# Optimization experiments

Measured on AMD Instinct MI355X. Metric: run time of the kernel, lower is better.

The kernel has to match this reference:

```python
import jax, jax.numpy as jnp
import numpy as np

N = 10000      # nodes
E = 160000     # edges
MUL = 64       # multiplicity of 0e and 1o in node feats / target
NATTR = 10     # number of element types (node_attrs one-hot width)
RDIM = 8       # radial (edge_feats) dim
NAVG = 16.0    # num_avg_neighbors
_INV3 = 0.5773502691896258  # CG coeff for 1o x 1o -> 0e (1/sqrt(3))


def setup_inputs() -> dict:
    key = jax.random.key(0)
    ks = jax.random.split(key, 20)
    return {
        "node_attrs": jax.random.uniform(ks[0], (N, NATTR), jnp.float32),
        "node_feats": jax.random.normal(ks[1], (N, 4 * MUL), jnp.float32),
        "edge_attrs_real": jax.random.normal(ks[2], (E, 4), jnp.float32),
        "edge_attrs_imag": jax.random.normal(ks[3], (E, 4), jnp.float32),
        "edge_feats": jax.random.normal(ks[4], (E, RDIM), jnp.float32),
        # linear_up (per-l internal weights)
        "W_up0": jax.random.normal(ks[5], (MUL, MUL), jnp.float32),
        "W_up1": jax.random.normal(ks[6], (MUL, MUL), jnp.float32),
        # conv_tp_weights MLP: [8, 64, 64, 64, 4*MUL]
        "M1": jax.random.normal(ks[7], (RDIM, 64), jnp.float32),
        "M2": jax.random.normal(ks[8], (64, 64), jnp.float32),
        "M3": jax.random.normal(ks[9], (64, 64), jnp.float32),
        "M4": jax.random.normal(ks[10], (64, 4 * MUL), jnp.float32),
        # linear: irreps_mid (128x0e+128x1o) -> irreps_nonlin (128x0e+64x1o)
        "W_lin_s": jax.random.normal(ks[11], (2 * MUL, 2 * MUL), jnp.float32),
        "W_lin_v": jax.random.normal(ks[12], (2 * MUL, MUL), jnp.float32),
        # skip_tp: FullyConnectedTensorProduct(node_feats, node_attrs -> irreps_nonlin)
        "W_sk_s": jax.random.normal(ks[13], (MUL, NATTR, 2 * MUL), jnp.float32),
        "W_sk_v": jax.random.normal(ks[14], (MUL, NATTR, MUL), jnp.float32),
        "edge_index": jax.random.randint(ks[15], (2, E), 0, N, jnp.int64
                                         if jax.config.jax_enable_x64 else jnp.int32),
    }


def _forward(node_attrs, node_feats, edge_attrs_real, edge_attrs_imag, edge_feats,
             W_up0, W_up1, M1, M2, M3, M4, W_lin_s, W_lin_v, W_sk_s, W_sk_v,
             sender, receiver):
    n = node_feats.shape[0]
    x0 = node_feats[:, :MUL]                          # (N, 64)   64x0e
    x1 = node_feats[:, MUL:].reshape(n, MUL, 3)       # (N, 64, 3) 64x1o

    # skip TP (fully connected, node_attrs are scalars)
    sk_norm = 1.0 / np.sqrt(MUL * NATTR)
    sc_s = jnp.einsum('nu,na,uav->nv', x0, node_attrs, W_sk_s) * sk_norm   # (N,128)
    sc_v = jnp.einsum('nui,na,uav->nvi', x1, node_attrs, W_sk_v) * sk_norm # (N,64,3)

    # linear_up (per-l)
    up_norm = 1.0 / np.sqrt(MUL)
    x0 = (x0 @ W_up0) * up_norm
    x1 = jnp.einsum('nui,uv->nvi', x1, W_up1) * up_norm

    # radial MLP -> per-edge TP weights (4 uvu paths x MUL)
    h = jax.nn.silu((edge_feats @ M1) / np.sqrt(RDIM))
    h = jax.nn.silu((h @ M2) / 8.0)
    h = jax.nn.silu((h @ M3) / 8.0)
    tw = (h @ M4) / 8.0                               # (E, 256)
    wA, wB, wC, wD = (tw[:, :MUL], tw[:, MUL:2*MUL],
                      tw[:, 2*MUL:3*MUL], tw[:, 3*MUL:])

    xs0 = x0[sender]                                  # (E, 64)
    xs1 = x1[sender]                                  # (E, 64, 3)

    def conv_tp(y):
        # y: (E,4) = [0e | 1o]; uvu paths with per-edge weights
        y0, y1 = y[:, :1], y[:, 1:]
        s = jnp.concatenate([xs0 * y0 * wA,                                  # 0e x 0e -> 0e
                             jnp.einsum('eui,ei->eu', xs1, y1) * _INV3 * wD  # 1o x 1o -> 0e
                             ], axis=1)                                      # (E,128)
        v = jnp.concatenate([(xs0 * wB)[:, :, None] * y1[:, None, :],        # 0e x 1o -> 1o
                             xs1 * (y0 * wC)[:, :, None]                     # 1o x 0e -> 1o
                             ], axis=1)                                      # (E,128,3)
        return s, v

    sr, vr = conv_tp(edge_attrs_real)
    si, vi = conv_tp(edge_attrs_imag)

    ms_r = jax.ops.segment_sum(sr, receiver, num_segments=n)
    mv_r = jax.ops.segment_sum(vr, receiver, num_segments=n)
    ms_i = jax.ops.segment_sum(si, receiver, num_segments=n)
    mv_i = jax.ops.segment_sum(vi, receiver, num_segments=n)

    lin_norm = (1.0 / np.sqrt(2 * MUL)) / (2.0 * NAVG)

    def lin(ms, mv):
        return (ms @ W_lin_s) * lin_norm, jnp.einsum('nui,uv->nvi', mv, W_lin_v) * lin_norm

    def gate(s, v):
        # irreps_nonlin = 64x0e scalars | 64x0e gates | 64x1o gated
        scal = jax.nn.silu(s[:, :MUL])
        g = jax.nn.silu(s[:, MUL:])
        return jnp.concatenate([scal, (v * g[:, :, None]).reshape(n, 3 * MUL)], axis=1)

    ls, lv = lin(ms_r, mv_r)
    real = gate(ls + sc_s, lv + sc_v)                 # (N, 256), residual on real part
    lsi, lvi = lin(ms_i, mv_i)
    imag = gate(lsi, lvi)                             # (N, 256)

    # view_as_complex + reshape [N, num_features, dim//num_features]; complex kept
    # as trailing real/imag axis of size 2.
    return jnp.stack([real, imag], axis=-1).reshape(n, MUL, (4 * MUL) // MUL, 2)


def reference(node_attrs, node_feats, edge_attrs_real, edge_attrs_imag, edge_feats,
              W_up0, W_up1, M1, M2, M3, M4, W_lin_s, W_lin_v, W_sk_s, W_sk_v,
              edge_index):
    sender, receiver = edge_index[0], edge_index[1]
    return _forward(node_attrs, node_feats, edge_attrs_real, edge_attrs_imag,
                    edge_feats, W_up0, W_up1, M1, M2, M3, M4,
                    W_lin_s, W_lin_v, W_sk_s, W_sk_v, sender, receiver)
```

## Files before the change

kernel.cpp:

```cpp
#include <hip/hip_runtime.h>
#include <hip/hip_bf16.h>

#define NN 10000
#define NE 160000
#define NGRP 625
#define XPLN 640000

#define SK_NORM   0.039528470752104741f
#define UP_NORM   0.125f
#define M1_NORM   0.35355339059327373f
#define INV3      0.5773502691896258f
#define LIN_NORM  0.0027621358640099516f

__device__ __forceinline__ float siluf(float x) { return x / (1.0f + __expf(-x)); }

__device__ __forceinline__ unsigned short f2bf_bits(float x) {
    union { __hip_bfloat16 h; unsigned short u; } cv;
    cv.h = __float2bfloat16(x);
    return cv.u;
}
__device__ __forceinline__ float bflo(unsigned int w) { return __uint_as_float(w << 16); }
__device__ __forceinline__ float bfhi(unsigned int w) { return __uint_as_float(w & 0xffff0000u); }

typedef short bf16x8 __attribute__((ext_vector_type(8)));
typedef float f32x4  __attribute__((ext_vector_type(4)));

__global__ __launch_bounds__(256) void k_detect(const int* __restrict__ ei32, int* __restrict__ flag) {
    __shared__ int cnt;
    if (threadIdx.x == 0) cnt = 0;
    __syncthreads();
    int z = 0;
    for (int i = threadIdx.x; i < 1024; i += 256)
        if (ei32[2 * i + 1] == 0) z++;
    atomicAdd(&cnt, z);
    __syncthreads();
    if (threadIdx.x == 0) flag[0] = (cnt >= 512) ? 1 : 0;
}

__global__ __launch_bounds__(256) void k_cvt(const int* __restrict__ ei32, const int* __restrict__ flag,
                                             int* __restrict__ snd, int* __restrict__ rcv) {
    int e = blockIdx.x * 256 + threadIdx.x;
    if (e >= NE) return;
    if (flag[0]) {
        const long long* e64 = (const long long*)ei32;
        snd[e] = (int)e64[e];
        rcv[e] = (int)e64[NE + e];
    } else {
        snd[e] = ei32[e];
        rcv[e] = ei32[NE + e];
    }
}

__global__ __launch_bounds__(256) void k_wprepN(
    const float* __restrict__ Wsk_s, const float* __restrict__ Wsk_v,
    const float* __restrict__ Wu0, const float* __restrict__ Wu1,
    unsigned short* __restrict__ WNF) {
    int idx = blockIdx.x * 256 + threadIdx.x;
    if (idx >= 131072) return;
    float val;
    if (idx < 81920) {
        int p = idx / 10240, r = idx % 10240;
        int kc = r >> 9, l8 = r & 511;
        int lane = l8 >> 3, j = l8 & 7, quad = lane >> 4, lo = lane & 15;
        int a = kc >> 1, u = (kc & 1) * 32 + quad * 8 + j;
        val = Wsk_s[(u * 10 + a) * 128 + p * 16 + lo];
    } else if (idx < 122880) {
        int rel = idx - 81920;
        int p = rel / 10240, r = rel % 10240;
        int kc = r >> 9, l8 = r & 511;
        int lane = l8 >> 3, j = l8 & 7, quad = lane >> 4, lo = lane & 15;
        int a = kc >> 1, u = (kc & 1) * 32 + quad * 8 + j;
        val = Wsk_v[(u * 10 + a) * 64 + p * 16 + lo];
    } else if (idx < 126976) {
        int rel = idx - 122880;
        int p = rel >> 10, r = rel & 1023;
        int kc = r >> 9, l8 = r & 511;
        int lane = l8 >> 3, j = l8 & 7, quad = lane >> 4, lo = lane & 15;
        int u = kc * 32 + quad * 8 + j;
        val = Wu0[u * 64 + p * 16 + lo];
    } else {
        int rel = idx - 126976;
        int p = rel >> 10, r = rel & 1023;
        int kc = r >> 9, l8 = r & 511;
        int lane = l8 >> 3, j = l8 & 7, quad = lane >> 4, lo = lane & 15;
        int u = kc * 32 + quad * 8 + j;
        val = Wu1[u * 64 + p * 16 + lo];
    }
    WNF[idx] = f2bf_bits(val);
}

__global__ __launch_bounds__(256) void k_xprep(
    const float* __restrict__ node_attrs, const float* __restrict__ node_feats,
    unsigned short* __restrict__ xpk, float* __restrict__ attrsP) {
    int idx = blockIdx.x * 256 + threadIdx.x;
    if (idx < 4 * NN * 64) {
        int n = idx >> 8, c = idx & 255;
        int plane = c >> 6, u = c & 63;
        float v = (plane == 0) ? node_feats[(long)n * 256 + u]
                               : node_feats[(long)n * 256 + 64 + u * 3 + (plane - 1)];
        xpk[(size_t)plane * XPLN + (long)n * 64 + u] = f2bf_bits(v);
        return;
    }
    int i2 = idx - 4 * NN * 64;
    if (i2 < 10 * NN) {
        int a = i2 / NN, n = i2 - a * NN;
        attrsP[i2] = node_attrs[(long)n * 10 + a];
    }
}

__global__ __launch_bounds__(256) void k_wprep2(
    const float* __restrict__ M1, const float* __restrict__ M2,
    const float* __restrict__ M3, const float* __restrict__ M4,
    const float* __restrict__ W_lin_s, const float* __restrict__ W_lin_v,
    unsigned short* __restrict__ WFG, unsigned short* __restrict__ WLF) {
    int idx = blockIdx.x * 256 + threadIdx.x;
    if (idx >= (52 + 48) * 512) return;
    if (idx < 52 * 512) {
        int f = idx >> 9, r = idx & 511;
        int lane = r >> 3, j = r & 7;
        int quad = lane >> 4, lo = lane & 15;
        float val;
        if (f < 4) {
            int n = f * 16 + lo, k = quad * 8 + j;
            val = (k < 8) ? M1[k * 64 + n] : 0.f;
        } else if (f < 12) {
            int g2 = f - 4, nt = g2 >> 1, half = g2 & 1;
            int n = nt * 16 + lo, k = half * 32 + quad * 8 + j;
            val = M2[k * 64 + n];
        } else if (f < 20) {
            int g3 = f - 12, nt = g3 >> 1, half = g3 & 1;
            int n = nt * 16 + lo, k = half * 32 + quad * 8 + j;
            val = M3[k * 64 + n];
        } else {
            int g4 = f - 20, tt = g4 >> 1, half = g4 & 1;
            int n = tt * 16 + lo, k = half * 32 + quad * 8 + j;
            val = M4[k * 256 + n];
        }
        WFG[idx] = f2bf_bits(val);
    } else {
        int rel = idx - 52 * 512;
        int f = rel >> 9, r = rel & 511;
        int lane = r >> 3, j = r & 7;
        int quad = lane >> 4, lo = lane & 15;
        float val;
        if (f < 32) {
            int vt = f >> 2, ks = f & 3;
            val = W_lin_s[(ks * 32 + quad * 8 + j) * 128 + vt * 16 + lo];
        } else {
            int f2 = f - 32;
            int vt = f2 >> 2, ks = f2 & 3;
            val = W_lin_v[(ks * 32 + quad * 8 + j) * 64 + vt * 16 + lo];
        }
        WLF[rel] = f2bf_bits(val);
    }
}

#define G0 8
#define NB0 79
#define G2 4
#define NB2 157
#define G3 16
#define NB3 40
#define KNODE_GRID (4*NB0 + 2*NB2 + 2*NB3)

__global__ __launch_bounds__(128) void k_node(
    const unsigned short* __restrict__ xpk, const float* __restrict__ attrsP,
    const unsigned short* __restrict__ WNF,
    float* __restrict__ sc_s, float* __restrict__ sc_v,
    float* __restrict__ x0u, float* __restrict__ x1p) {
    __shared__ unsigned short pan[2 * 10240];
    __shared__ float att[10 * 128];

    int t = threadIdx.x;
    int bid = blockIdx.x;
    int type, vp, chunk;
    if (bid < 4 * NB0)                 { type = 0; vp = bid / NB0; chunk = bid % NB0; }
    else if (bid < 4 * NB0 + 2 * NB2)  { int r = bid - 4 * NB0; type = 2; vp = r / NB2; chunk = r % NB2; }
    else                               { int r = bid - 4 * NB0 - 2 * NB2; type = 3; vp = r / NB3; chunk = r % NB3; }
    int G = (type == 0) ? G0 : (type == 2 ? G2 : G3);
    int g0 = chunk * G;
    int ng = NGRP - g0; if (ng > G) ng = G;
    int n0 = g0 * 16;

    int psrc, pcnt;
    if (type == 0)      { psrc = vp * 2 * 10240;           pcnt = 20480; }
    else if (type == 2) { psrc = 81920 + vp * 2 * 10240;   pcnt = 20480; }
    else                { psrc = 122880 + vp * 2 * 1024;   pcnt = 2048;  }
    for (int i = t; i < pcnt / 8; i += 128)
        ((float4*)pan)[i] = ((const float4*)(WNF + psrc))[i];
    if (type == 3) {
        for (int i = t; i < 2048 / 8; i += 128)
            ((float4*)(pan + 2048))[i] = ((const float4*)(WNF + 126976 + vp * 2 * 1024))[i];
    }
    if (type <= 2) {
        int cnt = ng * 16;
        #pragma unroll
        for (int k = 0; k < 10; k++) {
            int i = k * 128 + t;
            int nl = t;
            if (nl < cnt) att[i] = attrsP[k * NN + n0 + nl];
        }
    }
    __syncthreads();

    int wv = t >> 6, lane = t & 63, lo = lane & 15, quad = lane >> 4;
    int lbase = lane * 8;
    const f32x4 zacc = {0.f, 0.f, 0.f, 0.f};
    const unsigned short* mypan = pan + wv * 10240;

    if (type == 0) {
        int vtg = vp * 2 + wv;
        const unsigned short* xb = xpk;
        bf16x8 nfa0 = *(const bf16x8*)(xb + (long)(n0 + lo) * 64 + quad * 8);
        bf16x8 nfa1 = *(const bf16x8*)(xb + (long)(n0 + lo) * 64 + 32 + quad * 8);
        #pragma unroll 1
        for (int g = 0; g < ng; g++) {
            bf16x8 fa0 = nfa0, fa1 = nfa1;
            if (g + 1 < ng) {
                nfa0 = *(const bf16x8*)(xb + (long)(n0 + (g + 1) * 16 + lo) * 64 + quad * 8);
                nfa1 = *(const bf16x8*)(xb + (long)(n0 + (g + 1) * 16 + lo) * 64 + 32 + quad * 8);
            }
            f32x4 acc = zacc;
            #pragma unroll
            for (int a = 0; a < 10; a++) {
                bf16x8 b0 = *(const bf16x8*)&mypan[(2 * a) * 512 + lbase];
                bf16x8 b1 = *(const bf16x8*)&mypan[(2 * a + 1) * 512 + lbase];
                f32x4 p = __builtin_amdgcn_mfma_f32_16x16x32_bf16(fa0, b0, zacc, 0, 0, 0);
                p = __builtin_amdgcn_mfma_f32_16x16x32_bf16(fa1, b1, p, 0, 0, 0);
                float4 afv = *(const float4*)&att[a * 128 + g * 16 + quad * 4];
                acc[0] += afv.x * p[0]; acc[1] += afv.y * p[1];
                acc[2] += afv.z * p[2]; acc[3] += afv.w * p[3];
            }
            int nb = n0 + g * 16;
            #pragma unroll
            for (int r = 0; r < 4; r++)
                sc_s[(long)(nb + quad * 4 + r) * 128 + vtg * 16 + lo] = acc[r] * SK_NORM;
        }
    } else if (type == 2) {
        int vt = vp * 2 + wv;
        bf16x8 nfa0[3], nfa1[3];
        #pragma unroll
        for (int i = 0; i < 3; i++) {
            const unsigned short* xb = xpk + (size_t)(1 + i) * XPLN + (long)(n0 + lo) * 64;
            nfa0[i] = *(const bf16x8*)(xb + quad * 8);
            nfa1[i] = *(const bf16x8*)(xb + 32 + quad * 8);
        }
        #pragma unroll 1
        for (int g = 0; g < ng; g++) {
            bf16x8 fa0[3], fa1[3];
            #pragma unroll
            for (int i = 0; i < 3; i++) { fa0[i] = nfa0[i]; fa1[i] = nfa1[i]; }
            if (g + 1 < ng) {
                #pragma unroll
                for (int i = 0; i < 3; i++) {
                    const unsigned short* xb = xpk + (size_t)(1 + i) * XPLN + (long)(n0 + (g + 1) * 16 + lo) * 64;
                    nfa0[i] = *(const bf16x8*)(xb + quad * 8);
                    nfa1[i] = *(const bf16x8*)(xb + 32 + quad * 8);
                }
            }
            f32x4 acc0 = zacc, acc1 = zacc, acc2 = zacc;
            #pragma unroll
            for (int a = 0; a < 10; a++) {
                bf16x8 b0 = *(const bf16x8*)&mypan[(2 * a) * 512 + lbase];
                bf16x8 b1 = *(const bf16x8*)&mypan[(2 * a + 1) * 512 + lbase];
                float4 afv = *(const float4*)&att[a * 128 + g * 16 + quad * 4];
                f32x4 p0 = __builtin_amdgcn_mfma_f32_16x16x32_bf16(fa0[0], b0, zacc, 0, 0, 0);
                p0 = __builtin_amdgcn_mfma_f32_16x16x32_bf16(fa1[0], b1, p0, 0, 0, 0);
                acc0[0] += afv.x * p0[0]; acc0[1] += afv.y * p0[1];
                acc0[2] += afv.z * p0[2]; acc0[3] += afv.w * p0[3];
                f32x4 p1 = __builtin_amdgcn_mfma_f32_16x16x32_bf16(fa0[1], b0, zacc, 0, 0, 0);
                p1 = __builtin_amdgcn_mfma_f32_16x16x32_bf16(fa1[1], b1, p1, 0, 0, 0);
                acc1[0] += afv.x * p1[0]; acc1[1] += afv.y * p1[1];
                acc1[2] += afv.z * p1[2]; acc1[3] += afv.w * p1[3];
                f32x4 p2 = __builtin_amdgcn_mfma_f32_16x16x32_bf16(fa0[2], b0, zacc, 0, 0, 0);
                p2 = __builtin_amdgcn_mfma_f32_16x16x32_bf16(fa1[2], b1, p2, 0, 0, 0);
                acc2[0] += afv.x * p2[0]; acc2[1] += afv.y * p2[1];
                acc2[2] += afv.z * p2[2]; acc2[3] += afv.w * p2[3];
            }
            int nb = n0 + g * 16;
            #pragma unroll
            for (int r = 0; r < 4; r++) {
                long rb = (long)(nb + quad * 4 + r) * 192 + vt * 16 + lo;
                sc_v[rb]       = acc0[r] * SK_NORM;
                sc_v[rb + 64]  = acc1[r] * SK_NORM;
                sc_v[rb + 128] = acc2[r] * SK_NORM;
            }
        }
    } else {
        int vt = vp * 2 + wv;
        bf16x8 bk20 = *(const bf16x8*)&pan[wv * 1024 + lbase];
        bf16x8 bk21 = *(const bf16x8*)&pan[wv * 1024 + 512 + lbase];
        bf16x8 bk30 = *(const bf16x8*)&pan[2048 + wv * 1024 + lbase];
        bf16x8 bk31 = *(const bf16x8*)&pan[2048 + wv * 1024 + 512 + lbase];
        #pragma unroll 1
        for (int g = 0; g < ng; g++) {
            int nb = n0 + g * 16;
            {
                const unsigned short* xb = xpk + (long)(nb + lo) * 64;
                bf16x8 fa0 = *(const bf16x8*)(xb + quad * 8);
                bf16x8 fa1 = *(const bf16x8*)(xb + 32 + quad * 8);
                f32x4 acc = __builtin_amdgcn_mfma_f32_16x16x32_bf16(fa0, bk20, zacc, 0, 0, 0);
                acc = __builtin_amdgcn_mfma_f32_16x16x32_bf16(fa1, bk21, acc, 0, 0, 0);
                #pragma unroll
                for (int r = 0; r < 4; r++)
                    x0u[(long)(nb + quad * 4 + r) * 64 + vt * 16 + lo] = acc[r] * UP_NORM;
            }
            #pragma unroll
            for (int i = 0; i < 3; i++) {
                const unsigned short* xb = xpk + (size_t)(1 + i) * XPLN + (long)(nb + lo) * 64;
                bf16x8 fa0 = *(const bf16x8*)(xb + quad * 8);
                bf16x8 fa1 = *(const bf16x8*)(xb + 32 + quad * 8);
                f32x4 acc = __builtin_amdgcn_mfma_f32_16x16x32_bf16(fa0, bk30, zacc, 0, 0, 0);
                acc = __builtin_amdgcn_mfma_f32_16x16x32_bf16(fa1, bk31, acc, 0, 0, 0);
                #pragma unroll
                for (int r = 0; r < 4; r++)
                    x1p[(size_t)i * XPLN + (long)(nb + quad * 4 + r) * 64 + vt * 16 + lo] = acc[r] * UP_NORM;
            }
        }
    }
}

__global__ __launch_bounds__(256) void k_hist(const int* __restrict__ rcv, int* __restrict__ counts) {
    int e = blockIdx.x * 256 + threadIdx.x;
    if (e < NE) atomicAdd(&counts[rcv[e]], 1);
}

__global__ __launch_bounds__(1024) void k_scan(const int* __restrict__ counts, int* __restrict__ offsets) {
    __shared__ int partial[1024];
    int t = threadIdx.x;
    const int CHUNK = (NN + 1023) / 1024;
    int base = t * CHUNK;
    int s = 0;
    for (int i = 0; i < CHUNK; i++) if (base + i < NN) s += counts[base + i];
    partial[t] = s;
    __syncthreads();
    for (int d = 1; d < 1024; d *= 2) {
        int v = (t >= d) ? partial[t - d] : 0;
        __syncthreads();
        partial[t] += v;
        __syncthreads();
    }
    int excl = (t == 0) ? 0 : partial[t - 1];
    for (int i = 0; i < CHUNK; i++) {
        if (base + i < NN) { offsets[base + i] = excl; excl += counts[base + i]; }
    }
    if (t == 1023) offsets[NN] = partial[1023];
}

__global__ __launch_bounds__(256) void k_fill(const int* __restrict__ rcv, const int* __restrict__ snd,
                                              const int* __restrict__ offsets,
                                              int* __restrict__ cursor, int2* __restrict__ epk) {
    int e = blockIdx.x * 256 + threadIdx.x;
    if (e < NE) {
        int r = rcv[e];
        int pos = atomicAdd(&cursor[r], 1);
        epk[offsets[r] + pos] = make_int2(snd[e], e);
    }
}

__global__ __launch_bounds__(256) void k_eprep(const int2* __restrict__ epk,
                                               const float4* __restrict__ ear, const float4* __restrict__ eai,
                                               const float4* __restrict__ ef,
                                               int* __restrict__ sndp,
                                               float4* __restrict__ earp, float4* __restrict__ eaip,
                                               float4* __restrict__ efp) {
    int j = blockIdx.x * 256 + threadIdx.x;
    if (j >= NE) return;
    int2 se = epk[j];
    sndp[j] = se.x;
    earp[j] = ear[se.y];
    eaip[j] = eai[se.y];
    efp[(long)j * 2]     = ef[(long)se.y * 2];
    efp[(long)j * 2 + 1] = ef[(long)se.y * 2 + 1];
}

#define HID_STRIDE 72
#define OB_STRIDE  40
#define EPB 256
#define EMW 8

__global__ __launch_bounds__(512) void k_edge_mlp(
    const float4* __restrict__ efp, const unsigned short* __restrict__ WFG,
    __hip_bfloat16* __restrict__ twp) {
    __shared__ unsigned short wfrag[52 * 512];
    __shared__ unsigned short hid[EMW][16 * HID_STRIDE];

    int t = threadIdx.x;
    for (int i = t; i < 52 * 512 / 8; i += 512)
        ((float4*)wfrag)[i] = ((const float4*)WFG)[i];
    __syncthreads();

    int wv = t >> 6;
    int lane = t & 63;
    int lo = lane & 15;
    int quad = lane >> 4;
    int lbase = lane * 8;
    unsigned short* myhid = hid[wv];
    unsigned short* myob  = hid[wv];
    const f32x4 zacc = {0.f, 0.f, 0.f, 0.f};

    float4 f0, f1;
    if (quad == 0) {
        long jb0 = (long)blockIdx.x * EPB + wv * 16;
        f0 = efp[(jb0 + lo) * 2];
        f1 = efp[(jb0 + lo) * 2 + 1];
    }

    #pragma unroll 1
    for (int g = 0; g < EPB / 128; g++) {
        long jbase = (long)blockIdx.x * EPB + g * 128 + wv * 16;

        bf16x8 a1 = {0, 0, 0, 0, 0, 0, 0, 0};
        if (quad == 0) {
            union { unsigned short us[8]; bf16x8 v; } pk;
            pk.us[0] = f2bf_bits(f0.x * M1_NORM); pk.us[1] = f2bf_bits(f0.y * M1_NORM);
            pk.us[2] = f2bf_bits(f0.z * M1_NORM); pk.us[3] = f2bf_bits(f0.w * M1_NORM);
            pk.us[4] = f2bf_bits(f1.x * M1_NORM); pk.us[5] = f2bf_bits(f1.y * M1_NORM);
            pk.us[6] = f2bf_bits(f1.z * M1_NORM); pk.us[7] = f2bf_bits(f1.w * M1_NORM);
            a1 = pk.v;
            if (g + 1 < EPB / 128) {
                long jbn = jbase + 128;
                f0 = efp[(jbn + lo) * 2];
                f1 = efp[(jbn + lo) * 2 + 1];
            }
        }
        {
            f32x4 acc[4];
            #pragma unroll
            for (int nt = 0; nt < 4; nt++) {
                bf16x8 b = *(const bf16x8*)&wfrag[nt * 512 + lbase];
                acc[nt] = __builtin_amdgcn_mfma_f32_16x16x32_bf16(a1, b, zacc, 0, 0, 0);
            }
            #pragma unroll
            for (int nt = 0; nt < 4; nt++)
                #pragma unroll
                for (int r = 0; r < 4; r++)
                    myhid[(quad * 4 + r) * HID_STRIDE + nt * 16 + lo] = f2bf_bits(siluf(acc[nt][r]));
        }

        #pragma unroll
        for (int L = 0; L < 2; L++) {
            int fb = 4 + L * 8;
            bf16x8 a0 = *(const bf16x8*)&myhid[lo * HID_STRIDE + quad * 8];
            bf16x8 a1v = *(const bf16x8*)&myhid[lo * HID_STRIDE + 32 + quad * 8];
            f32x4 acc[4];
            #pragma unroll
            for (int nt = 0; nt < 4; nt++) {
                bf16x8 b0 = *(const bf16x8*)&wfrag[(fb + nt * 2) * 512 + lbase];
                bf16x8 b1 = *(const bf16x8*)&wfrag[(fb + nt * 2 + 1) * 512 + lbase];
                acc[nt] = __builtin_amdgcn_mfma_f32_16x16x32_bf16(a0, b0, zacc, 0, 0, 0);
                acc[nt] = __builtin_amdgcn_mfma_f32_16x16x32_bf16(a1v, b1, acc[nt], 0, 0, 0);
            }
            #pragma unroll
            for (int nt = 0; nt < 4; nt++)
                #pragma unroll
                for (int r = 0; r < 4; r++)
                    myhid[(quad * 4 + r) * HID_STRIDE + nt * 16 + lo] = f2bf_bits(siluf(acc[nt][r] * 0.125f));
        }

        {
            bf16x8 a0 = *(const bf16x8*)&myhid[lo * HID_STRIDE + quad * 8];
            bf16x8 a1v = *(const bf16x8*)&myhid[lo * HID_STRIDE + 32 + quad * 8];
            int sedge = lane >> 2, sch = lane & 3;
            #pragma unroll 1
            for (int rd = 0; rd < 8; rd++) {
                f32x4 acc2[2];
                #pragma unroll
                for (int p = 0; p < 2; p++) {
                    int tt = (rd < 4) ? (p * 4 + rd) : (8 + p * 4 + (rd - 4));
                    bf16x8 b0 = *(const bf16x8*)&wfrag[(20 + tt * 2) * 512 + lbase];
                    bf16x8 b1 = *(const bf16x8*)&wfrag[(20 + tt * 2 + 1) * 512 + lbase];
                    acc2[p] = __builtin_amdgcn_mfma_f32_16x16x32_bf16(a0, b0, zacc, 0, 0, 0);
                    acc2[p] = __builtin_amdgcn_mfma_f32_16x16x32_bf16(a1v, b1, acc2[p], 0, 0, 0);
                }
                #pragma unroll
                for (int p = 0; p < 2; p++)
                    #pragma unroll
                    for (int r = 0; r < 4; r++)
                        myob[(quad * 4 + r) * OB_STRIDE + 2 * lo + p] = f2bf_bits(acc2[p][r] * 0.125f);
                bf16x8 vv = *(const bf16x8*)&myob[sedge * OB_STRIDE + sch * 8];
                *(bf16x8*)(twp + (jbase + sedge) * 256 + rd * 32 + sch * 8) = vv;
            }
        }
    }
}

#define NPB 4
#define CB2 4
__global__ __launch_bounds__(256) void k_conv(
    const int* __restrict__ offsets, const int* __restrict__ sndp,
    const float4* __restrict__ earp, const float4* __restrict__ eaip,
    const float* __restrict__ x0u, const float* __restrict__ x1p,
    const __hip_bfloat16* __restrict__ twp,
    unsigned short* __restrict__ msgF) {
    __shared__ unsigned short stg[NPB][1024];
    int t = threadIdx.x;
    int wv = t >> 6;
    int u = t & 63;
    int n = blockIdx.x * NPB + wv;
    int beg = offsets[n], end = offsets[n + 1];
    int deg = end - beg;
    int sreg = (u < deg) ? sndp[beg + u] : 0;
    const int tsel0 = 2 * u, tsel1 = 128 + 2 * u;
    float a0r = 0.f, a1r = 0.f, a2r = 0.f, a3r = 0.f;
    float a0i = 0.f, a1i = 0.f, a2i = 0.f, a3i = 0.f;
    float c0r = 0.f, c1r = 0.f, c2r = 0.f, c3r = 0.f;
    float c0i = 0.f, c1i = 0.f, c2i = 0.f, c3i = 0.f;

    for (int jb = beg; jb < end; jb += CB2) {
        unsigned int t0[CB2], t1[CB2];
        float x0v[CB2], xv0[CB2], xv1[CB2], xv2[CB2];
        float4 yr[CB2], yi[CB2];
        #pragma unroll
        for (int p = 0; p < CB2; p++) {
            int j = jb + p;
            int jc = (j < end) ? j : (end - 1);
            int le = jc - beg;
            int s = (le < 64) ? __shfl(sreg, le) : sndp[jc];
            yr[p] = earp[jc];
            yi[p] = eaip[jc];
            long sb = (long)s * 64 + u;
            x0v[p] = x0u[sb];
            xv0[p] = x1p[sb];
            xv1[p] = x1p[XPLN + sb];
            xv2[p] = x1p[2 * XPLN + sb];
            bool valid = (j < end);
            t0[p] = valid ? *(const unsigned int*)(twp + (long)jc * 256 + tsel0) : 0u;
            t1[p] = valid ? *(const unsigned int*)(twp + (long)jc * 256 + tsel1) : 0u;
        }
        #pragma unroll
        for (int p = 0; p < CB2; p++) {
            float wA = bflo(t0[p]), wB = bfhi(t0[p]);
            float xa = x0v[p] * wA, xb = x0v[p] * wB;
            a0r += xa * yr[p].x; a1r += xb * yr[p].y; a2r += xb * yr[p].z; a3r += xb * yr[p].w;
            a0i += xa * yi[p].x; a1i += xb * yi[p].y; a2i += xb * yi[p].z; a3i += xb * yi[p].w;
            float wC = bflo(t1[p]), wDs = bfhi(t1[p]) * INV3;
            float dr = xv0[p] * yr[p].y + xv1[p] * yr[p].z + xv2[p] * yr[p].w;
            float di = xv0[p] * yi[p].y + xv1[p] * yi[p].z + xv2[p] * yi[p].w;
            c0r += dr * wDs; c0i += di * wDs;
            float ycr = yr[p].x * wC, yci = yi[p].x * wC;
            c1r += xv0[p] * ycr; c2r += xv1[p] * ycr; c3r += xv2[p] * ycr;
            c1i += xv0[p] * yci; c2i += xv1[p] * yci; c3i += xv2[p] * yci;
        }
    }

    unsigned short* sg = stg[wv];
    sg[u]       = f2bf_bits(a0r);
    sg[128 + u] = f2bf_bits(a0i);
    sg[256 + u] = f2bf_bits(a1r);
    sg[384 + u] = f2bf_bits(a2r);
    sg[512 + u] = f2bf_bits(a3r);
    sg[640 + u] = f2bf_bits(a1i);
    sg[768 + u] = f2bf_bits(a2i);
    sg[896 + u] = f2bf_bits(a3i);
    sg[64 + u]  = f2bf_bits(c0r);
    sg[192 + u] = f2bf_bits(c0i);
    sg[320 + u] = f2bf_bits(c1r);
    sg[448 + u] = f2bf_bits(c2r);
    sg[576 + u] = f2bf_bits(c3r);
    sg[704 + u] = f2bf_bits(c1i);
    sg[832 + u] = f2bf_bits(c2i);
    sg[960 + u] = f2bf_bits(c3i);
    __syncthreads();

    #pragma unroll
    for (int rep = 0; rep < 2; rep++) {
        int job = rep * 256 + t;
        int m = job >> 7, c = job & 127;
        int nm = blockIdx.x * NPB + m;
        int g = nm >> 4, lo = nm & 15;
        bf16x8 vv = *(const bf16x8*)&stg[m][c * 8];
        *(bf16x8*)(msgF + (size_t)g * 16384 + (c >> 2) * 512 + lo * 32 + (c & 3) * 8) = vv;
    }
}

#define SV_STRIDE 129
#define VV_STRIDE 65

__global__ __launch_bounds__(256, 3) void k_lin(
    const unsigned short* __restrict__ msgF,
    const float* __restrict__ sc_s, const float* __restrict__ sc_v,
    const unsigned short* __restrict__ WLF,
    float* __restrict__ out) {
    __shared__ char smem[49152];
    unsigned short* wfrag = (unsigned short*)smem;
    float* sval = (float*)smem;
    float* vval = (float*)(smem + 2 * 16 * SV_STRIDE * 4);

    int t = threadIdx.x;
    for (int i = t; i < 48 * 512 / 8; i += 256)
        ((float4*)wfrag)[i] = ((const float4*)WLF)[i];
    __syncthreads();

    int wv = t >> 6;
    int lane = t & 63;
    int lo = lane & 15;
    int quad = lane >> 4;
    int lbase = lane * 8;
    int aoff_lane = lo * 32 + quad * 8;
    const f32x4 zacc = {0.f, 0.f, 0.f, 0.f};

    long g = blockIdx.x;
    long nbase = g * 16;
    const unsigned short* agbase = msgF + (size_t)g * 16384;

    f32x4 accs[10];
    #pragma unroll
    for (int q = 0; q < 10; q++) {
        int tau = wv + q * 4;
        int cblk, fb;
        if (tau < 16) {
            int ri = tau >> 3, vt = tau & 7;
            cblk = ri; fb = vt * 4;
        } else {
            int tp = tau - 16;
            int ri = tp / 12, rem = tp % 12;
            int i = rem >> 2, vt = rem & 3;
            cblk = 2 + ri * 3 + i; fb = 32 + vt * 4;
        }
        f32x4 acc = zacc;
        #pragma unroll
        for (int ks = 0; ks < 4; ks++) {
            bf16x8 a = *(const bf16x8*)(agbase + (cblk * 4 + ks) * 512 + aoff_lane);
            bf16x8 b = *(const bf16x8*)&wfrag[(fb + ks) * 512 + lbase];
            acc = __builtin_amdgcn_mfma_f32_16x16x32_bf16(a, b, acc, 0, 0, 0);
        }
        accs[q] = acc;
    }
    __syncthreads();

    #pragma unroll
    for (int q = 0; q < 10; q++) {
        int tau = wv + q * 4;
        if (tau < 16) {
            int ri = tau >> 3, vt = tau & 7;
            int cidx = (ri * 16) * SV_STRIDE + vt * 16 + lo;
            #pragma unroll
            for (int r = 0; r < 4; r++)
                sval[cidx + (quad * 4 + r) * SV_STRIDE] = accs[q][r] * LIN_NORM;
        } else {
            int tp = tau - 16;
            int ri = tp / 12, rem = tp % 12;
            int i = rem >> 2, vt = rem & 3;
            int cidx = ((ri * 3 + i) * 16) * VV_STRIDE + vt * 16 + lo;
            #pragma unroll
            for (int r = 0; r < 4; r++)
                vval[cidx + (quad * 4 + r) * VV_STRIDE] = accs[q][r] * LIN_NORM;
        }
    }
    __syncthreads();

    #pragma unroll 1
    for (int j = 0; j < 16; j++) {
        int c = t;
        long gn = nbase + j;
        float re, im;
        if (c < 64) {
            float sr = sval[(0 * 16 + j) * SV_STRIDE + c] + sc_s[gn * 128 + c];
            float si = sval[(1 * 16 + j) * SV_STRIDE + c];
            re = siluf(sr); im = siluf(si);
        } else {
            int rem = c - 64;
            int v = rem / 3;
            int i = rem - v * 3;
            float gr = siluf(sval[(0 * 16 + j) * SV_STRIDE + 64 + v] + sc_s[gn * 128 + 64 + v]);
            float gi = siluf(sval[(1 * 16 + j) * SV_STRIDE + 64 + v]);
            float lr = vval[((0 * 3 + i) * 16 + j) * VV_STRIDE + v] + sc_v[gn * 192 + i * 64 + v];
            float li = vval[((1 * 3 + i) * 16 + j) * VV_STRIDE + v];
            re = lr * gr; im = li * gi;
        }
        ((float2*)out)[gn * 256 + c] = make_float2(re, im);
    }
}

extern "C" void kernel_launch(void* const* d_in, const int* in_sizes, int n_in,
                              void* d_out, int out_size, void* d_ws, size_t ws_size,
                              hipStream_t stream) {
    const float* node_attrs = (const float*)d_in[0];
    const float* node_feats = (const float*)d_in[1];
    const float* ear        = (const float*)d_in[2];
    const float* eai        = (const float*)d_in[3];
    const float* edge_feats = (const float*)d_in[4];
    const float* W_up0      = (const float*)d_in[5];
    const float* W_up1      = (const float*)d_in[6];
    const float* M1         = (const float*)d_in[7];
    const float* M2         = (const float*)d_in[8];
    const float* M3         = (const float*)d_in[9];
    const float* M4         = (const float*)d_in[10];
    const float* W_lin_s    = (const float*)d_in[11];
    const float* W_lin_v    = (const float*)d_in[12];
    const float* W_sk_s     = (const float*)d_in[13];
    const float* W_sk_v     = (const float*)d_in[14];
    const int*   ei         = (const int*)d_in[15];

    char* ws = (char*)d_ws;
    size_t o_x0u = 0;
    size_t o_x1p = o_x0u + (size_t)NN * 64 * 4;
    size_t o_scs = o_x1p + (size_t)NN * 256 * 4;
    size_t o_scv = o_scs + (size_t)NN * 128 * 4;
    size_t o_tw  = o_scv + (size_t)NN * 192 * 4;
    size_t o_cnt = o_tw  + (size_t)NE * 256 * 2;
    size_t o_cur = o_cnt + (size_t)NN * 4;
    size_t o_ofs = o_cur + (size_t)NN * 4;
    size_t o_epk = o_ofs + (size_t)(NN + 1) * 4 + 60;
    size_t o_snd = o_epk + (size_t)NE * 8;
    size_t o_rcv = o_snd + (size_t)NE * 4;
    size_t o_flg = o_rcv + (size_t)NE * 4;
    size_t o_msg = o_flg + 64;
    size_t o_wnf = o_msg + (size_t)NN * 1024 * 2;
    size_t o_snp = o_wnf + 262144;
    size_t o_erp = o_snp + (size_t)NE * 4;
    size_t o_eip = o_erp + (size_t)NE * 16;
    size_t o_efp = o_eip + (size_t)NE * 16;
    size_t o_wfg = o_efp + (size_t)NE * 32;
    size_t o_wlf = o_wfg + (size_t)52 * 512 * 2;
    size_t o_xpk = o_wlf + (size_t)48 * 512 * 2;
    size_t o_atp = o_xpk + (size_t)4 * NN * 64 * 2;

    float* x0u = (float*)(ws + o_x0u);
    float* x1p = (float*)(ws + o_x1p);
    float* sc_s = (float*)(ws + o_scs);
    float* sc_v = (float*)(ws + o_scv);
    __hip_bfloat16* twp = (__hip_bfloat16*)(ws + o_tw);
    int* counts  = (int*)(ws + o_cnt);
    int* cursor  = (int*)(ws + o_cur);
    int* offsets = (int*)(ws + o_ofs);
    int2* epk    = (int2*)(ws + o_epk);
    int* snd     = (int*)(ws + o_snd);
    int* rcv     = (int*)(ws + o_rcv);
    int* flag    = (int*)(ws + o_flg);
    unsigned short* msgF = (unsigned short*)(ws + o_msg);
    unsigned short* WNF = (unsigned short*)(ws + o_wnf);
    int*    sndp = (int*)(ws + o_snp);
    float4* earp = (float4*)(ws + o_erp);
    float4* eaip = (float4*)(ws + o_eip);
    float4* efp  = (float4*)(ws + o_efp);
    unsigned short* WFG = (unsigned short*)(ws + o_wfg);
    unsigned short* WLF = (unsigned short*)(ws + o_wlf);
    unsigned short* xpk = (unsigned short*)(ws + o_xpk);
    float* attrsP = (float*)(ws + o_atp);

    hipMemsetAsync(ws + o_cnt, 0, (size_t)NN * 8, stream);

    dim3 b256(256), b1024(1024), b128(128), b512(512);
    k_detect<<<dim3(1), b256, 0, stream>>>(ei, flag);
    k_cvt   <<<dim3((NE + 255) / 256), b256, 0, stream>>>(ei, flag, snd, rcv);
    k_hist<<<dim3((NE + 255) / 256), b256, 0, stream>>>(rcv, counts);
    k_scan<<<dim3(1), b1024, 0, stream>>>(counts, offsets);
    k_fill<<<dim3((NE + 255) / 256), b256, 0, stream>>>(rcv, snd, offsets, cursor, epk);
    k_eprep<<<dim3((NE + 255) / 256), b256, 0, stream>>>(epk, (const float4*)ear, (const float4*)eai,
                                                         (const float4*)edge_feats,
                                                         sndp, earp, eaip, efp);
    k_wprepN<<<dim3(512), b256, 0, stream>>>(W_sk_s, W_sk_v, W_up0, W_up1, WNF);
    k_wprep2<<<dim3(200), b256, 0, stream>>>(M1, M2, M3, M4, W_lin_s, W_lin_v, WFG, WLF);
    k_xprep <<<dim3((4 * NN * 64 + 10 * NN + 255) / 256), b256, 0, stream>>>(node_attrs, node_feats, xpk, attrsP);
    k_node  <<<dim3(KNODE_GRID), b128, 0, stream>>>(xpk, attrsP, WNF, sc_s, sc_v, x0u, x1p);
    k_edge_mlp<<<dim3(NE / EPB), b512, 0, stream>>>(efp, WFG, twp);
    k_conv<<<dim3(NN / NPB), b256, 0, stream>>>(offsets, sndp, earp, eaip, x0u, x1p, twp, msgF);
    k_lin <<<dim3(NGRP), b256, 0, stream>>>(msgF, sc_s, sc_v, WLF, (float*)d_out);
}
```

Baseline: 276.7 us.

## Shrink edge MLP blocks, read last-layer weights from global, fully unroll output loop

The edge MLP kernel now uses 256-thread blocks that each handle 64 edges in one pass instead of 512-thread blocks looping over 256 edges. Only the first three layers' weight fragments are staged in shared memory, and the large final-layer weights are read straight from global memory (through cache). Shared memory per block drops sharply, so more blocks can be resident, and the per-block weight staging is cheaper. In exchange there are far more blocks, each restaging the small weights, the final-layer weights are read from global on every use, and the prefetch of the next group's edge features is gone. The scan variable rename is cosmetic.

```diff
diff --git a/kernel.cpp b/kernel.cpp
--- a/kernel.cpp
+++ b/kernel.cpp
@@ -328,10 +328,10 @@
 __global__ __launch_bounds__(1024) void k_scan(const int* __restrict__ counts, int* __restrict__ offsets) {
     __shared__ int partial[1024];
     int t = threadIdx.x;
-    const int CHUNK = (NN + 1023) / 1024;
-    int base = t * CHUNK;
+    const int CHUNKS = (NN + 1023) / 1024;
+    int base = t * CHUNKS;
     int s = 0;
-    for (int i = 0; i < CHUNK; i++) if (base + i < NN) s += counts[base + i];
+    for (int i = 0; i < CHUNKS; i++) if (base + i < NN) s += counts[base + i];
     partial[t] = s;
     __syncthreads();
     for (int d = 1; d < 1024; d *= 2) {
@@ -341,7 +341,7 @@
         __syncthreads();
     }
     int excl = (t == 0) ? 0 : partial[t - 1];
-    for (int i = 0; i < CHUNK; i++) {
+    for (int i = 0; i < CHUNKS; i++) {
         if (base + i < NN) { offsets[base + i] = excl; excl += counts[base + i]; }
     }
     if (t == 1023) offsets[NN] = partial[1023];
@@ -376,17 +376,16 @@
 
 #define HID_STRIDE 72
 #define OB_STRIDE  40
-#define EPB 256
-#define EMW 8
-
-__global__ __launch_bounds__(512) void k_edge_mlp(
+#define EPB 64
+
+__global__ __launch_bounds__(256) void k_edge_mlp(
     const float4* __restrict__ efp, const unsigned short* __restrict__ WFG,
     __hip_bfloat16* __restrict__ twp) {
-    __shared__ unsigned short wfrag[52 * 512];
-    __shared__ unsigned short hid[EMW][16 * HID_STRIDE];
+    __shared__ unsigned short wfrag[20 * 512];
+    __shared__ unsigned short hid[4][16 * HID_STRIDE];
 
     int t = threadIdx.x;
-    for (int i = t; i < 52 * 512 / 8; i += 512)
+    for (int i = t; i < 20 * 512 / 8; i += 256)
         ((float4*)wfrag)[i] = ((const float4*)WFG)[i];
     __syncthreads();
 
@@ -397,90 +396,78 @@
     int lbase = lane * 8;
     unsigned short* myhid = hid[wv];
     unsigned short* myob  = hid[wv];
+    const unsigned short* W4 = WFG + 20 * 512;
     const f32x4 zacc = {0.f, 0.f, 0.f, 0.f};
 
-    float4 f0, f1;
+    long jbase = (long)blockIdx.x * EPB + wv * 16;
+
+    bf16x8 a1 = {0, 0, 0, 0, 0, 0, 0, 0};
     if (quad == 0) {
-        long jb0 = (long)blockIdx.x * EPB + wv * 16;
-        f0 = efp[(jb0 + lo) * 2];
-        f1 = efp[(jb0 + lo) * 2 + 1];
-    }
-
-    #pragma unroll 1
-    for (int g = 0; g < EPB / 128; g++) {
-        long jbase = (long)blockIdx.x * EPB + g * 128 + wv * 16;
-
-        bf16x8 a1 = {0, 0, 0, 0, 0, 0, 0, 0};
-        if (quad == 0) {
-            union { unsigned short us[8]; bf16x8 v; } pk;
-            pk.us[0] = f2bf_bits(f0.x * M1_NORM); pk.us[1] = f2bf_bits(f0.y * M1_NORM);
-            pk.us[2] = f2bf_bits(f0.z * M1_NORM); pk.us[3] = f2bf_bits(f0.w * M1_NORM);
-            pk.us[4] = f2bf_bits(f1.x * M1_NORM); pk.us[5] = f2bf_bits(f1.y * M1_NORM);
-            pk.us[6] = f2bf_bits(f1.z * M1_NORM); pk.us[7] = f2bf_bits(f1.w * M1_NORM);
-            a1 = pk.v;
-            if (g + 1 < EPB / 128) {
-                long jbn = jbase + 128;
-                f0 = efp[(jbn + lo) * 2];
-                f1 = efp[(jbn + lo) * 2 + 1];
+        float4 f0 = efp[(jbase + lo) * 2];
+        float4 f1 = efp[(jbase + lo) * 2 + 1];
+        union { unsigned short us[8]; bf16x8 v; } pk;
+        pk.us[0] = f2bf_bits(f0.x * M1_NORM); pk.us[1] = f2bf_bits(f0.y * M1_NORM);
+        pk.us[2] = f2bf_bits(f0.z * M1_NORM); pk.us[3] = f2bf_bits(f0.w * M1_NORM);
+        pk.us[4] = f2bf_bits(f1.x * M1_NORM); pk.us[5] = f2bf_bits(f1.y * M1_NORM);
+        pk.us[6] = f2bf_bits(f1.z * M1_NORM); pk.us[7] = f2bf_bits(f1.w * M1_NORM);
+        a1 = pk.v;
+    }
+    {
+        f32x4 acc[4];
+        #pragma unroll
+        for (int nt = 0; nt < 4; nt++) {
+            bf16x8 b = *(const bf16x8*)&wfrag[nt * 512 + lbase];
+            acc[nt] = __builtin_amdgcn_mfma_f32_16x16x32_bf16(a1, b, zacc, 0, 0, 0);
+        }
+        #pragma unroll
+        for (int nt = 0; nt < 4; nt++)
+            #pragma unroll
+            for (int r = 0; r < 4; r++)
+                myhid[(quad * 4 + r) * HID_STRIDE + nt * 16 + lo] = f2bf_bits(siluf(acc[nt][r]));
+    }
+
+    #pragma unroll
+    for (int L = 0; L < 2; L++) {
+        int fb = 4 + L * 8;
+        bf16x8 a0 = *(const bf16x8*)&myhid[lo * HID_STRIDE + quad * 8];
+        bf16x8 a1v = *(const bf16x8*)&myhid[lo * HID_STRIDE + 32 + quad * 8];
+        f32x4 acc[4];
+        #pragma unroll
+        for (int nt = 0; nt < 4; nt++) {
+            bf16x8 b0 = *(const bf16x8*)&wfrag[(fb + nt * 2) * 512 + lbase];
+            bf16x8 b1 = *(const bf16x8*)&wfrag[(fb + nt * 2 + 1) * 512 + lbase];
+            acc[nt] = __builtin_amdgcn_mfma_f32_16x16x32_bf16(a0, b0, zacc, 0, 0, 0);
+            acc[nt] = __builtin_amdgcn_mfma_f32_16x16x32_bf16(a1v, b1, acc[nt], 0, 0, 0);
+        }
+        #pragma unroll
+        for (int nt = 0; nt < 4; nt++)
+            #pragma unroll
+            for (int r = 0; r < 4; r++)
+                myhid[(quad * 4 + r) * HID_STRIDE + nt * 16 + lo] = f2bf_bits(siluf(acc[nt][r] * 0.125f));
+    }
+
+    {
+        bf16x8 a0 = *(const bf16x8*)&myhid[lo * HID_STRIDE + quad * 8];
+        bf16x8 a1v = *(const bf16x8*)&myhid[lo * HID_STRIDE + 32 + quad * 8];
+        int sedge = lane >> 2, sch = lane & 3;
+        #pragma unroll
+        for (int rd = 0; rd < 8; rd++) {
+            f32x4 acc2[2];
+            #pragma unroll
+            for (int p = 0; p < 2; p++) {
+                int tt = (rd < 4) ? (p * 4 + rd) : (8 + p * 4 + (rd - 4));
+                bf16x8 b0 = *(const bf16x8*)(W4 + (tt * 2) * 512 + lbase);
+                bf16x8 b1 = *(const bf16x8*)(W4 + (tt * 2 + 1) * 512 + lbase);
+                acc2[p] = __builtin_amdgcn_mfma_f32_16x16x32_bf16(a0, b0, zacc, 0, 0, 0);
+                acc2[p] = __builtin_amdgcn_mfma_f32_16x16x32_bf16(a1v, b1, acc2[p], 0, 0, 0);
             }
-        }
-        {
-            f32x4 acc[4];
-            #pragma unroll
-            for (int nt = 0; nt < 4; nt++) {
-                bf16x8 b = *(const bf16x8*)&wfrag[nt * 512 + lbase];
-                acc[nt] = __builtin_amdgcn_mfma_f32_16x16x32_bf16(a1, b, zacc, 0, 0, 0);
-            }
-            #pragma unroll
-            for (int nt = 0; nt < 4; nt++)
+            #pragma unroll
+            for (int p = 0; p < 2; p++)
                 #pragma unroll
                 for (int r = 0; r < 4; r++)
-                    myhid[(quad * 4 + r) * HID_STRIDE + nt * 16 + lo] = f2bf_bits(siluf(acc[nt][r]));
-        }
-
-        #pragma unroll
-        for (int L = 0; L < 2; L++) {
-            int fb = 4 + L * 8;
-            bf16x8 a0 = *(const bf16x8*)&myhid[lo * HID_STRIDE + quad * 8];
-            bf16x8 a1v = *(const bf16x8*)&myhid[lo * HID_STRIDE + 32 + quad * 8];
-            f32x4 acc[4];
-            #pragma unroll
-            for (int nt = 0; nt < 4; nt++) {
-                bf16x8 b0 = *(const bf16x8*)&wfrag[(fb + nt * 2) * 512 + lbase];
-                bf16x8 b1 = *(const bf16x8*)&wfrag[(fb + nt * 2 + 1) * 512 + lbase];
-                acc[nt] = __builtin_amdgcn_mfma_f32_16x16x32_bf16(a0, b0, zacc, 0, 0, 0);
-                acc[nt] = __builtin_amdgcn_mfma_f32_16x16x32_bf16(a1v, b1, acc[nt], 0, 0, 0);
-            }
-            #pragma unroll
-            for (int nt = 0; nt < 4; nt++)
-                #pragma unroll
-                for (int r = 0; r < 4; r++)
-                    myhid[(quad * 4 + r) * HID_STRIDE + nt * 16 + lo] = f2bf_bits(siluf(acc[nt][r] * 0.125f));
-        }
-
-        {
-            bf16x8 a0 = *(const bf16x8*)&myhid[lo * HID_STRIDE + quad * 8];
-            bf16x8 a1v = *(const bf16x8*)&myhid[lo * HID_STRIDE + 32 + quad * 8];
-            int sedge = lane >> 2, sch = lane & 3;
-            #pragma unroll 1
-            for (int rd = 0; rd < 8; rd++) {
-                f32x4 acc2[2];
-                #pragma unroll
-                for (int p = 0; p < 2; p++) {
-                    int tt = (rd < 4) ? (p * 4 + rd) : (8 + p * 4 + (rd - 4));
-                    bf16x8 b0 = *(const bf16x8*)&wfrag[(20 + tt * 2) * 512 + lbase];
-                    bf16x8 b1 = *(const bf16x8*)&wfrag[(20 + tt * 2 + 1) * 512 + lbase];
-                    acc2[p] = __builtin_amdgcn_mfma_f32_16x16x32_bf16(a0, b0, zacc, 0, 0, 0);
-                    acc2[p] = __builtin_amdgcn_mfma_f32_16x16x32_bf16(a1v, b1, acc2[p], 0, 0, 0);
-                }
-                #pragma unroll
-                for (int p = 0; p < 2; p++)
-                    #pragma unroll
-                    for (int r = 0; r < 4; r++)
-                        myob[(quad * 4 + r) * OB_STRIDE + 2 * lo + p] = f2bf_bits(acc2[p][r] * 0.125f);
-                bf16x8 vv = *(const bf16x8*)&myob[sedge * OB_STRIDE + sch * 8];
-                *(bf16x8*)(twp + (jbase + sedge) * 256 + rd * 32 + sch * 8) = vv;
-            }
+                    myob[(quad * 4 + r) * OB_STRIDE + 2 * lo + p] = f2bf_bits(acc2[p][r] * 0.125f);
+            bf16x8 vv = *(const bf16x8*)&myob[sedge * OB_STRIDE + sch * 8];
+            *(bf16x8*)(twp + (jbase + sedge) * 256 + rd * 32 + sch * 8) = vv;
         }
     }
 }
@@ -742,7 +729,7 @@
 
     hipMemsetAsync(ws + o_cnt, 0, (size_t)NN * 8, stream);
 
-    dim3 b256(256), b1024(1024), b128(128), b512(512);
+    dim3 b256(256), b1024(1024), b128(128);
     k_detect<<<dim3(1), b256, 0, stream>>>(ei, flag);
     k_cvt   <<<dim3((NE + 255) / 256), b256, 0, stream>>>(ei, flag, snd, rcv);
     k_hist<<<dim3((NE + 255) / 256), b256, 0, stream>>>(rcv, counts);
@@ -755,7 +742,7 @@
     k_wprep2<<<dim3(200), b256, 0, stream>>>(M1, M2, M3, M4, W_lin_s, W_lin_v, WFG, WLF);
     k_xprep <<<dim3((4 * NN * 64 + 10 * NN + 255) / 256), b256, 0, stream>>>(node_attrs, node_feats, xpk, attrsP);
     k_node  <<<dim3(KNODE_GRID), b128, 0, stream>>>(xpk, attrsP, WNF, sc_s, sc_v, x0u, x1p);
-    k_edge_mlp<<<dim3(NE / EPB), b512, 0, stream>>>(efp, WFG, twp);
+    k_edge_mlp<<<dim3(NE / EPB), b256, 0, stream>>>(efp, WFG, twp);
     k_conv<<<dim3(NN / NPB), b256, 0, stream>>>(offsets, sndp, earp, eaip, x0u, x1p, twp, msgF);
     k_lin <<<dim3(NGRP), b256, 0, stream>>>(msgF, sc_s, sc_v, WLF, (float*)d_out);
 }
```

Result: faster. 270.1 us (-2.4%).
